# Kernel tuning notes

Measured on AMD Instinct MI355X. Metric: run time of the kernel, lower is better.

## Reference

```python
import jax, jax.numpy as jnp
import numpy as np

B, L, INPUT_DIM = 4, 4096, 32
D_MODEL, N_LAYERS = 256, 2
D_STATE, D_CONV, EXPAND = 16, 4, 2
D_INNER = EXPAND * D_MODEL          # 512
DT_RANK = (D_MODEL + 15) // 16      # 16
OUTPUT_DIM, HORIZON = 32, 4
LN_EPS = 1e-5


def setup_inputs() -> dict:
    key = jax.random.key(0)
    ks = jax.random.split(key, 16)
    s = 0.02
    inp = {
        "x": jax.random.normal(ks[0], (B, L, INPUT_DIM), jnp.float32),
        "enc_w": jax.random.normal(ks[1], (D_MODEL, INPUT_DIM), jnp.float32) * s,
        "enc_b": jnp.zeros((D_MODEL,), jnp.float32),
        "in_proj_w": jax.random.normal(ks[2], (N_LAYERS, 2 * D_INNER, D_MODEL), jnp.float32) * s,
        "conv_w": jax.random.normal(ks[3], (N_LAYERS, D_INNER, D_CONV), jnp.float32) * s,
        "conv_b": jnp.zeros((N_LAYERS, D_INNER), jnp.float32),
        "xproj_w": jax.random.normal(ks[4], (N_LAYERS, DT_RANK + 2 * D_STATE, D_INNER), jnp.float32) * s,
        "dtproj_w": jax.random.normal(ks[5], (N_LAYERS, D_INNER, DT_RANK), jnp.float32) * s,
        "dtproj_b": jax.random.normal(ks[6], (N_LAYERS, D_INNER), jnp.float32) * 0.1,
        "A_log": jnp.log(jnp.tile(jnp.arange(1.0, D_STATE + 1.0, dtype=jnp.float32), (N_LAYERS, D_INNER, 1))),
        "Dp": jnp.ones((N_LAYERS, D_INNER), jnp.float32),
        "out_proj_w": jax.random.normal(ks[7], (N_LAYERS, D_MODEL, D_INNER), jnp.float32) * s,
        "ln_g": jnp.ones((D_MODEL,), jnp.float32),
        "ln_b": jnp.zeros((D_MODEL,), jnp.float32),
        "head_w": jax.random.normal(ks[8], (OUTPUT_DIM * HORIZON, D_MODEL), jnp.float32) * s,
        "head_b": jnp.zeros((OUTPUT_DIM * HORIZON,), jnp.float32),
    }
    return inp


def _mamba_block(x, in_w, cw, cb, xp_w, dt_w, dt_b, A_log, Dp, out_w):
    # x: [B, L, d_model]
    b, l, _ = x.shape
    xz = jnp.einsum("bld,ed->ble", x, in_w)            # [B, L, 2*d_inner]
    xi, res = jnp.split(xz, 2, axis=-1)
    # causal depthwise conv1d (padding=d_conv-1, truncated to L)
    xpad = jnp.pad(xi, ((0, 0), (D_CONV - 1, 0), (0, 0)))
    xi = sum(xpad[:, k:k + l, :] * cw[:, k] for k in range(D_CONV)) + cb
    xi = jax.nn.silu(xi)
    dbl = jnp.einsum("bld,ed->ble", xi, xp_w)           # [B, L, dt_rank+2*d_state]
    dt = dbl[..., :DT_RANK]
    Bm = dbl[..., DT_RANK:DT_RANK + D_STATE]            # [B, L, d_state]
    Cm = dbl[..., DT_RANK + D_STATE:]                   # [B, L, d_state]
    dt = jax.nn.softplus(jnp.einsum("blr,dr->bld", dt, dt_w) + dt_b)  # [B, L, d_inner]
    A = -jnp.exp(A_log)                                 # [d_inner, d_state]

    def step(h, ins):
        dt_t, B_t, C_t, x_t = ins                       # [B,di],[B,ds],[B,ds],[B,di]
        dA = jnp.exp(dt_t[..., None] * A)               # [B, d_inner, d_state]
        h = dA * h + (dt_t * x_t)[..., None] * B_t[:, None, :]
        y = jnp.einsum("bds,bs->bd", h, C_t)
        return h, y

    h0 = jnp.zeros((b, D_INNER, D_STATE), x.dtype)
    xs = (jnp.moveaxis(dt, 1, 0), jnp.moveaxis(Bm, 1, 0),
          jnp.moveaxis(Cm, 1, 0), jnp.moveaxis(xi, 1, 0))
    _, ys = jax.lax.scan(step, h0, xs)                  # ys: [L, B, d_inner]
    y = jnp.moveaxis(ys, 0, 1) + xi * Dp
    y = y * jax.nn.silu(res)
    return jnp.einsum("ble,de->bld", y, out_w)


def reference(x, enc_w, enc_b, in_proj_w, conv_w, conv_b, xproj_w, dtproj_w,
              dtproj_b, A_log, Dp, out_proj_w, ln_g, ln_b, head_w, head_b):
    h = jnp.einsum("bli,di->bld", x, enc_w) + enc_b     # encoder
    for i in range(N_LAYERS):
        h = h + _mamba_block(h, in_proj_w[i], conv_w[i], conv_b[i], xproj_w[i],
                             dtproj_w[i], dtproj_b[i], A_log[i], Dp[i], out_proj_w[i])
    mu = jnp.mean(h, axis=-1, keepdims=True)
    var = jnp.mean((h - mu) ** 2, axis=-1, keepdims=True)
    hn = (h - mu) * jax.lax.rsqrt(var + LN_EPS) * ln_g + ln_b
    state = hn[:, -1, :]                                # last timestep
    return jnp.einsum("bd,od->bo", state, head_w) + head_b
```

## Files before the change

kernel.cpp:

```cpp
#include <hip/hip_runtime.h>
#include <hip/hip_bf16.h>
#include <math.h>

#define BB 4
#define LL 4096
#define DM 256
#define DI 512
#define DS 16
#define NOUTK 128
#define LN_EPS 1e-5f
#define NC 128
#define CLEN (LL/NC)
#define BL (BB*LL)
#define LDB 640

typedef __attribute__((ext_vector_type(8))) short short8;
typedef __attribute__((ext_vector_type(4))) float f32x4;

__device__ __forceinline__ ushort f2bf(float f) {
    union { float f; unsigned u; } v; v.f = f;
    unsigned r = (v.u + 0x7FFF + ((v.u >> 16) & 1)) >> 16;
    return (ushort)r;
}
__device__ __forceinline__ float bf2f(ushort u) {
    union { unsigned u; float f; } v; v.u = ((unsigned)u) << 16;
    return v.f;
}

#define PREP_N1 (2*1024*256)
#define PREP_N2 (2*256*512)
#define PREP_N3 (2*640*512)
#define PREP_BLOCKS ((PREP_N1 + PREP_N2 + PREP_N3) / 256)
#define ENC_BLOCKS (BL / 4)
__global__ __launch_bounds__(256) void prep_enc_kernel(
    const float* __restrict__ inw, const float* __restrict__ opw,
    const float* __restrict__ xpw, const float* __restrict__ dtw,
    ushort* __restrict__ inw_bf, ushort* __restrict__ opw_bf,
    ushort* __restrict__ comb_bf,
    const float* __restrict__ x, const float* __restrict__ encw,
    const float* __restrict__ encb, ushort* __restrict__ hbf)
{
    int tid = threadIdx.x;
    if (blockIdx.x < PREP_BLOCKS) {
        int i = blockIdx.x * 256 + tid;
        if (i < PREP_N1) {
            inw_bf[i] = f2bf(inw[i]);
            return;
        }
        int j = i - PREP_N1;
        if (j < PREP_N2) {
            opw_bf[j] = f2bf(opw[j]);
            return;
        }
        int m = j - PREP_N2;
        if (m >= PREP_N3) return;
        int l = m / (640 * 512);
        int rem = m - l * 640 * 512;
        int row = rem >> 9, k = rem & 511;
        const float* xp = xpw + l * 48 * 512;
        const float* dw = dtw + l * 512 * 16;
        float v;
        if (row < 512) {
            v = 0.f;
            #pragma unroll
            for (int r = 0; r < 16; ++r)
                v = fmaf(dw[row * 16 + r], xp[r * 512 + k], v);
        } else if (row < 544) {
            v = xp[(row - 512 + 16) * 512 + k];
        } else v = 0.f;
        comb_bf[m] = f2bf(v);
        return;
    }
    __shared__ float sw[256 * 33];
    __shared__ float sx[4][32];
    for (int i = tid; i < 256 * 8; i += 256) {
        float4 v = ((const float4*)encw)[i];
        int r = i >> 3, c = (i & 7) * 4;
        sw[r * 33 + c + 0] = v.x; sw[r * 33 + c + 1] = v.y;
        sw[r * 33 + c + 2] = v.z; sw[r * 33 + c + 3] = v.w;
    }
    int row0 = (blockIdx.x - PREP_BLOCKS) * 4;
    if (tid < 32) {
        for (int rr = 0; rr < 4; ++rr)
            sx[rr][tid] = x[(size_t)(row0 + rr) * 32 + tid];
    }
    __syncthreads();
    float bb = encb[tid];
    #pragma unroll
    for (int rr = 0; rr < 4; ++rr) {
        float acc = bb;
        #pragma unroll
        for (int k = 0; k < 32; ++k)
            acc = fmaf(sx[rr][k], sw[tid * 33 + k], acc);
        hbf[(size_t)(row0 + rr) * DM + tid] = f2bf(acc);
    }
}

template<int EPI>
__global__ __launch_bounds__(256, 4) void mfma_gemm(
    const ushort* __restrict__ A, int lda,
    const ushort* __restrict__ W,
    const float* __restrict__ bias,
    float* __restrict__ C, int ldc,
    ushort* Cbf, int ldcbf,
    int K)
{
    __shared__ ushort As[64 * 64];
    __shared__ ushort Ws[128 * 64];
    const int tid = threadIdx.x;

    int nwg = gridDim.x * gridDim.y;
    int wlin = blockIdx.y * gridDim.x + blockIdx.x;
    int gx = blockIdx.x, gy = blockIdx.y;
    if ((nwg & 7) == 0) {
        int q = nwg >> 3;
        int s = (wlin & 7) * q + (wlin >> 3);
        gx = s % gridDim.x;
        gy = s / gridDim.x;
    }
    const int bm = gy * 64;
    const int bn = gx * 128;
    const int wid = tid >> 6, lane = tid & 63;
    const int wrow = (wid >> 1) * 32, wcol = (wid & 1) * 64;
    const int sr = tid >> 3;
    const int sc = tid & 7;

    f32x4 acc[2][4];
    #pragma unroll
    for (int mi = 0; mi < 2; ++mi)
        #pragma unroll
        for (int ni = 0; ni < 4; ++ni)
            acc[mi][ni] = (f32x4){0.f, 0.f, 0.f, 0.f};

    const int nk = K >> 6;
    for (int t = 0; t < nk; ++t) {
        const int k0 = t << 6;
        #pragma unroll
        for (int it = 0; it < 2; ++it) {
            int r = it * 32 + sr;
            int csrc = sc ^ (r & 7);
            __builtin_amdgcn_global_load_lds(
                (const __attribute__((address_space(1))) unsigned int*)
                    (A + (size_t)(bm + r) * lda + k0 + csrc * 8),
                (__attribute__((address_space(3))) unsigned int*)
                    (As + r * 64 + sc * 8), 16, 0, 0);
        }
        #pragma unroll
        for (int it = 0; it < 4; ++it) {
            int r = it * 32 + sr;
            int csrc = sc ^ (r & 7);
            __builtin_amdgcn_global_load_lds(
                (const __attribute__((address_space(1))) unsigned int*)
                    (W + (size_t)(bn + r) * K + k0 + csrc * 8),
                (__attribute__((address_space(3))) unsigned int*)
                    (Ws + r * 64 + sc * 8), 16, 0, 0);
        }
        __syncthreads();
        #pragma unroll
        for (int kk = 0; kk < 2; ++kk) {
            short8 af[2], bfr[4];
            #pragma unroll
            for (int mi = 0; mi < 2; ++mi) {
                int r = wrow + mi * 16 + (lane & 15);
                int c = (lane >> 4) + kk * 4;
                af[mi] = *(const short8*)(As + r * 64 + ((c ^ (r & 7)) << 3));
            }
            #pragma unroll
            for (int ni = 0; ni < 4; ++ni) {
                int r = wcol + ni * 16 + (lane & 15);
                int c = (lane >> 4) + kk * 4;
                bfr[ni] = *(const short8*)(Ws + r * 64 + ((c ^ (r & 7)) << 3));
            }
            #pragma unroll
            for (int mi = 0; mi < 2; ++mi)
                #pragma unroll
                for (int ni = 0; ni < 4; ++ni)
                    acc[mi][ni] = __builtin_amdgcn_mfma_f32_16x16x32_bf16(
                        af[mi], bfr[ni], acc[mi][ni], 0, 0, 0);
        }
        __syncthreads();
    }

    #pragma unroll
    for (int mi = 0; mi < 2; ++mi)
        #pragma unroll
        for (int ni = 0; ni < 4; ++ni) {
            int col = bn + wcol + ni * 16 + (lane & 15);
            #pragma unroll
            for (int r = 0; r < 4; ++r) {
                int row = bm + wrow + mi * 16 + (lane >> 4) * 4 + r;
                float v = acc[mi][ni][r];
                if (EPI == 1) {
                    if (col < 512) {
                        float u = v + bias[col];
                        float sp = fmaxf(u, 0.f) + __logf(1.f + __expf(-fabsf(u)));
                        Cbf[(size_t)row * ldcbf + col] = f2bf(sp);
                    } else if (col < 544) {
                        C[(size_t)row * ldc + (col - 512)] = v;
                    }
                } else if (EPI == 2) {
                    size_t o = (size_t)row * ldcbf + col;
                    float vv = v + bf2f(Cbf[o]);
                    Cbf[o] = f2bf(vv);
                } else {
                    Cbf[(size_t)row * ldcbf + col] = f2bf(v);
                }
            }
        }
}

__global__ __launch_bounds__(256) void conv_silu_kernel(
    const ushort* __restrict__ xz, const float* __restrict__ cw,
    const float* __restrict__ cb, ushort* __restrict__ xi)
{
    int idx = blockIdx.x * 256 + threadIdx.x;
    int d4 = (idx & 127) * 4;
    int grp = idx >> 7;
    int b = grp >> 9;
    int t0 = (grp & 511) * 8;
    const ushort* base = xz + ((size_t)(b * LL + t0) * 1024) + d4;
    ushort* obase = xi + ((size_t)(b * LL + t0) * 512) + d4;

    float4 w0 = *(const float4*)(cw + (d4 + 0) * 4);
    float4 w1 = *(const float4*)(cw + (d4 + 1) * 4);
    float4 w2 = *(const float4*)(cw + (d4 + 2) * 4);
    float4 w3 = *(const float4*)(cw + (d4 + 3) * 4);
    float b0 = cb[d4 + 0], b1 = cb[d4 + 1], b2 = cb[d4 + 2], b3 = cb[d4 + 3];

    ushort4 z4 = {0, 0, 0, 0};
    ushort4 win0 = (t0 >= 3) ? *(const ushort4*)(base - 3 * 1024) : z4;
    ushort4 win1 = (t0 >= 2) ? *(const ushort4*)(base - 2 * 1024) : z4;
    ushort4 win2 = (t0 >= 1) ? *(const ushort4*)(base - 1 * 1024) : z4;

    #pragma unroll
    for (int k = 0; k < 8; ++k) {
        ushort4 cur = *(const ushort4*)(base + k * 1024);
        float a0 = b0, a1 = b1, a2 = b2, a3 = b3;
        a0 = fmaf(bf2f(win0.x), w0.x, a0); a1 = fmaf(bf2f(win0.y), w1.x, a1);
        a2 = fmaf(bf2f(win0.z), w2.x, a2); a3 = fmaf(bf2f(win0.w), w3.x, a3);
        a0 = fmaf(bf2f(win1.x), w0.y, a0); a1 = fmaf(bf2f(win1.y), w1.y, a1);
        a2 = fmaf(bf2f(win1.z), w2.y, a2); a3 = fmaf(bf2f(win1.w), w3.y, a3);
        a0 = fmaf(bf2f(win2.x), w0.z, a0); a1 = fmaf(bf2f(win2.y), w1.z, a1);
        a2 = fmaf(bf2f(win2.z), w2.z, a2); a3 = fmaf(bf2f(win2.w), w3.z, a3);
        a0 = fmaf(bf2f(cur.x),  w0.w, a0); a1 = fmaf(bf2f(cur.y),  w1.w, a1);
        a2 = fmaf(bf2f(cur.z),  w2.w, a2); a3 = fmaf(bf2f(cur.w),  w3.w, a3);
        ushort4 o;
        o.x = f2bf(a0 / (1.f + __expf(-a0)));
        o.y = f2bf(a1 / (1.f + __expf(-a1)));
        o.z = f2bf(a2 / (1.f + __expf(-a2)));
        o.w = f2bf(a3 / (1.f + __expf(-a3)));
        *(ushort4*)(obase + k * 512) = o;
        win0 = win1; win1 = win2; win2 = cur;
    }
}

__global__ __launch_bounds__(256) void scan_phase1(
    const ushort* __restrict__ xi, const ushort* __restrict__ dtb,
    const float* __restrict__ bc,
    const float* __restrict__ alog,
    float* __restrict__ cS, float* __restrict__ cH)
{
    int d = blockIdx.z * 256 + threadIdx.x;
    int b = blockIdx.y, c = blockIdx.x;
    float Av[16];
    bool fast = true;
    #pragma unroll
    for (int s = 0; s < 16; ++s) {
        Av[s] = -__expf(alog[d * 16 + s]);
        fast = fast && (fabsf(Av[s] + (float)(s + 1)) < 1e-3f * (s + 1));
    }
    float h[16];
    #pragma unroll
    for (int s = 0; s < 16; ++s) h[s] = 0.f;
    float S = 0.f;
    int t0 = c * CLEN;
    if (fast) {
        for (int t = t0; t < t0 + CLEN; ++t) {
            size_t row = (size_t)b * LL + t;
            float dt = bf2f(dtb[row * 512 + d]);
            float x = bf2f(xi[row * 512 + d]);
            float dtx = dt * x;
            S += dt;
            const float* bp = bc + row * 32;
            float e1 = __expf(-dt);
            float e2=e1*e1, e3=e2*e1, e4=e2*e2, e5=e3*e2, e6=e3*e3, e7=e4*e3, e8=e4*e4;
            float e9=e5*e4, e10=e5*e5, e11=e6*e5, e12=e6*e6, e13=e7*e6, e14=e7*e7, e15=e8*e7, e16=e8*e8;
            float pw[16] = {e1,e2,e3,e4,e5,e6,e7,e8,e9,e10,e11,e12,e13,e14,e15,e16};
            #pragma unroll
            for (int s = 0; s < 16; ++s)
                h[s] = fmaf(pw[s], h[s], dtx * bp[s]);
        }
    } else {
        for (int t = t0; t < t0 + CLEN; ++t) {
            size_t row = (size_t)b * LL + t;
            float dt = bf2f(dtb[row * 512 + d]);
            float x = bf2f(xi[row * 512 + d]);
            float dtx = dt * x;
            S += dt;
            const float* bp = bc + row * 32;
            #pragma unroll
            for (int s = 0; s < 16; ++s) {
                float dA = __expf(dt * Av[s]);
                h[s] = fmaf(dA, h[s], dtx * bp[s]);
            }
        }
    }
    cS[((size_t)b * DI + d) * NC + c] = S;
    size_t base = (((size_t)b * DI + d) * NC + c) * 16;
    #pragma unroll
    for (int q = 0; q < 4; ++q)
        *(float4*)(cH + base + q*4) = *(float4*)&h[q*4];
}

__global__ __launch_bounds__(256) void scan_phase2(
    const float* __restrict__ cS, float* __restrict__ cH,
    const float* __restrict__ alog)
{
    int bd = blockIdx.x;
    int d = bd & (DI - 1);
    int tid = threadIdx.x;
    int s = tid >> 4;
    int g = tid & 15;
    float Avs = -__expf(alog[d * 16 + s]);
    size_t sbase = (size_t)bd * NC;
    size_t base = (size_t)bd * NC * 16 + s;
    float a8[8], h8[8];
    #pragma unroll
    for (int j = 0; j < 8; ++j) {
        float Sj = cS[sbase + g * 8 + j];
        a8[j] = __expf(Avs * Sj);
        h8[j] = cH[base + (size_t)(g * 8 + j) * 16];
    }
    float A = 1.f, H = 0.f;
    #pragma unroll
    for (int j = 0; j < 8; ++j) {
        H = fmaf(a8[j], H, h8[j]);
        A *= a8[j];
    }
    #pragma unroll
    for (int off = 1; off < 16; off <<= 1) {
        float Ap = __shfl_up(A, off, 16);
        float Hp = __shfl_up(H, off, 16);
        if (g >= off) { H = fmaf(A, Hp, H); A *= Ap; }
    }
    float init = __shfl_up(H, 1, 16);
    if (g == 0) init = 0.f;
    #pragma unroll
    for (int j = 0; j < 8; ++j) {
        size_t o = base + (size_t)(g * 8 + j) * 16;
        cH[o] = init;
        init = fmaf(a8[j], init, h8[j]);
    }
}

__global__ __launch_bounds__(256) void scan_phase3(
    const ushort* __restrict__ xz,
    ushort* __restrict__ xi,
    const ushort* __restrict__ dtb,
    const float* __restrict__ bc,
    const float* __restrict__ alog,
    const float* __restrict__ Dp,
    const float* __restrict__ cH,
    int c0)
{
    int d = blockIdx.z * 256 + threadIdx.x;
    int b = blockIdx.y;
    int c = blockIdx.x + c0;
    float Av[16];
    bool fast = true;
    #pragma unroll
    for (int s = 0; s < 16; ++s) {
        Av[s] = -__expf(alog[d * 16 + s]);
        fast = fast && (fabsf(Av[s] + (float)(s + 1)) < 1e-3f * (s + 1));
    }
    float h[16];
    size_t cbase = (((size_t)b * DI + d) * NC + c) * 16;
    #pragma unroll
    for (int q = 0; q < 4; ++q)
        *(float4*)&h[q*4] = *(const float4*)(cH + cbase + q*4);
    float Dd = Dp[d];
    int t0 = c * CLEN;
    if (fast) {
        for (int t = t0; t < t0 + CLEN; ++t) {
            size_t row = (size_t)b * LL + t;
            float dt = bf2f(dtb[row * 512 + d]);
            float x = bf2f(xi[row * 512 + d]);
            float dtx = dt * x;
            const float* bp = bc + row * 32;
            const float* cp = bc + row * 32 + 16;
            float e1 = __expf(-dt);
            float e2=e1*e1, e3=e2*e1, e4=e2*e2, e5=e3*e2, e6=e3*e3, e7=e4*e3, e8=e4*e4;
            float e9=e5*e4, e10=e5*e5, e11=e6*e5, e12=e6*e6, e13=e7*e6, e14=e7*e7, e15=e8*e7, e16=e8*e8;
            float pw[16] = {e1,e2,e3,e4,e5,e6,e7,e8,e9,e10,e11,e12,e13,e14,e15,e16};
            float y = 0.f;
            #pragma unroll
            for (int s = 0; s < 16; ++s) {
                h[s] = fmaf(pw[s], h[s], dtx * bp[s]);
                y = fmaf(h[s], cp[s], y);
            }
            float res = bf2f(xz[row * 1024 + 512 + d]);
            float g = (y + x * Dd) * (res / (1.f + __expf(-res)));
            xi[row * 512 + d] = f2bf(g);
        }
    } else {
        for (int t = t0; t < t0 + CLEN; ++t) {
            size_t row = (size_t)b * LL + t;
            float dt = bf2f(dtb[row * 512 + d]);
            float x = bf2f(xi[row * 512 + d]);
            float dtx = dt * x;
            const float* bp = bc + row * 32;
            const float* cp = bc + row * 32 + 16;
            float y = 0.f;
            #pragma unroll
            for (int s = 0; s < 16; ++s) {
                float dA = __expf(dt * Av[s]);
                h[s] = fmaf(dA, h[s], dtx * bp[s]);
                y = fmaf(h[s], cp[s], y);
            }
            float res = bf2f(xz[row * 1024 + 512 + d]);
            float g = (y + x * Dd) * (res / (1.f + __expf(-res)));
            xi[row * 512 + d] = f2bf(g);
        }
    }
}

__global__ __launch_bounds__(256) void out_proj_last_kernel(
    const ushort* __restrict__ xi, const float* __restrict__ W,
    const ushort* __restrict__ hbf, float* __restrict__ hlast)
{
    int b = blockIdx.x, n = threadIdx.x;
    __shared__ float sy[DI];
    const ushort* yrow = xi + ((size_t)b * LL + (LL - 1)) * DI;
    for (int k = threadIdx.x; k < DI; k += 256) sy[k] = bf2f(yrow[k]);
    __syncthreads();
    const float* wr = W + (size_t)n * DI;
    float acc = 0.f;
    for (int k = 0; k < DI; k += 4) {
        float4 wv = *(const float4*)(wr + k);
        acc = fmaf(sy[k+0], wv.x, acc);
        acc = fmaf(sy[k+1], wv.y, acc);
        acc = fmaf(sy[k+2], wv.z, acc);
        acc = fmaf(sy[k+3], wv.w, acc);
    }
    hlast[b * DM + n] = acc + bf2f(hbf[((size_t)b * LL + (LL - 1)) * DM + n]);
}

__global__ __launch_bounds__(256) void ln_head_kernel(
    const float* __restrict__ hlast, const float* __restrict__ lng,
    const float* __restrict__ lnb, const float* __restrict__ hw,
    const float* __restrict__ hb, float* __restrict__ out)
{
    int b = blockIdx.x, tid = threadIdx.x;
    __shared__ float sh[DM];
    __shared__ float r1[4], r2[4];
    float v = hlast[b * DM + tid];
    float s = v;
    #pragma unroll
    for (int o = 32; o >= 1; o >>= 1) s += __shfl_down(s, o);
    if ((tid & 63) == 0) r1[tid >> 6] = s;
    __syncthreads();
    float mu = (r1[0] + r1[1] + r1[2] + r1[3]) * (1.f / 256.f);
    float dv = v - mu;
    float q = dv * dv;
    #pragma unroll
    for (int o = 32; o >= 1; o >>= 1) q += __shfl_down(q, o);
    if ((tid & 63) == 0) r2[tid >> 6] = q;
    __syncthreads();
    float var = (r2[0] + r2[1] + r2[2] + r2[3]) * (1.f / 256.f);
    sh[tid] = dv * rsqrtf(var + LN_EPS) * lng[tid] + lnb[tid];
    __syncthreads();
    if (tid < NOUTK) {
        const float* wr = hw + (size_t)tid * DM;
        float acc = hb[tid];
        for (int d2 = 0; d2 < DM; d2 += 4) {
            float4 wv = *(const float4*)(wr + d2);
            acc = fmaf(sh[d2+0], wv.x, acc);
            acc = fmaf(sh[d2+1], wv.y, acc);
            acc = fmaf(sh[d2+2], wv.z, acc);
            acc = fmaf(sh[d2+3], wv.w, acc);
        }
        out[b * NOUTK + tid] = acc;
    }
}

extern "C" void kernel_launch(void* const* d_in, const int* in_sizes, int n_in,
                              void* d_out, int out_size, void* d_ws, size_t ws_size,
                              hipStream_t stream)
{
    const float* x    = (const float*)d_in[0];
    const float* encw = (const float*)d_in[1];
    const float* encb = (const float*)d_in[2];
    const float* inw  = (const float*)d_in[3];
    const float* cw   = (const float*)d_in[4];
    const float* cb   = (const float*)d_in[5];
    const float* xpw  = (const float*)d_in[6];
    const float* dtw  = (const float*)d_in[7];
    const float* dtb  = (const float*)d_in[8];
    const float* alog = (const float*)d_in[9];
    const float* Dp   = (const float*)d_in[10];
    const float* opw  = (const float*)d_in[11];
    const float* lng  = (const float*)d_in[12];
    const float* lnb  = (const float*)d_in[13];
    const float* hw   = (const float*)d_in[14];
    const float* hb   = (const float*)d_in[15];
    float* out = (float*)d_out;

    float* ws   = (float*)d_ws;
    float* bc   = ws;
    float* cS   = bc  + (size_t)BL * 32;
    float* cH   = cS  + (size_t)BB * DI * NC;
    float* hlast = cH + (size_t)BB * DI * NC * DS;
    ushort* h_bf    = (ushort*)(hlast + BB * DM);
    ushort* xz_bf   = h_bf  + (size_t)BL * DM;
    ushort* xi_bf   = xz_bf + (size_t)BL * 1024;
    ushort* dt_bf   = xi_bf + (size_t)BL * DI;
    ushort* inw_bf  = dt_bf + (size_t)BL * DI;
    ushort* opw_bf  = inw_bf + 2 * 1024 * DM;
    ushort* comb_bf = opw_bf + 2 * DM * DI;

    dim3 blk(256, 1, 1);

    prep_enc_kernel<<<dim3(PREP_BLOCKS + ENC_BLOCKS), blk, 0, stream>>>(
        inw, opw, xpw, dtw, inw_bf, opw_bf, comb_bf,
        x, encw, encb, h_bf);

    for (int l = 0; l < 2; ++l) {
        mfma_gemm<0><<<dim3(1024/128, BL/64), blk, 0, stream>>>(
            h_bf, DM, inw_bf + (size_t)l * 1024 * DM, nullptr,
            nullptr, 0, xz_bf, 1024, DM);
        conv_silu_kernel<<<dim3(BL * 128 / 8 / 256), blk, 0, stream>>>(
            xz_bf, cw + l * DI * 4, cb + l * DI, xi_bf);
        mfma_gemm<1><<<dim3(LDB/128, BL/64), blk, 0, stream>>>(
            xi_bf, DI, comb_bf + (size_t)l * LDB * DI, dtb + l * DI,
            bc, 32, dt_bf, 512, DI);
        scan_phase1<<<dim3(NC, BB, 2), blk, 0, stream>>>(
            xi_bf, dt_bf, bc, alog + (size_t)l * DI * 16, cS, cH);
        scan_phase2<<<dim3(BB * DI), blk, 0, stream>>>(
            cS, cH, alog + (size_t)l * DI * 16);
        if (l == 0) {
            scan_phase3<<<dim3(NC, BB, 2), blk, 0, stream>>>(
                xz_bf, xi_bf, dt_bf, bc, alog + (size_t)l * DI * 16,
                Dp + l * DI, cH, 0);
            mfma_gemm<2><<<dim3(DM/128, BL/64), blk, 0, stream>>>(
                xi_bf, DI, opw_bf + (size_t)l * DM * DI, nullptr,
                nullptr, 0, h_bf, DM, DI);
        } else {
            scan_phase3<<<dim3(1, BB, 2), blk, 0, stream>>>(
                xz_bf, xi_bf, dt_bf, bc, alog + (size_t)l * DI * 16,
                Dp + l * DI, cH, NC - 1);
            out_proj_last_kernel<<<dim3(BB), blk, 0, stream>>>(
                xi_bf, opw + (size_t)l * DM * DI, h_bf, hlast);
        }
    }

    ln_head_kernel<<<dim3(BB), blk, 0, stream>>>(hlast, lng, lnb, hw, hb, out);
}
```

Baseline: 307.1 us.

## Unfuse dt low-rank projection: small x_proj GEMM plus separate dt combine

```diff
diff --git a/kernel.cpp b/kernel.cpp
--- a/kernel.cpp
+++ b/kernel.cpp
@@ -12,7 +12,6 @@
 #define NC 128
 #define CLEN (LL/NC)
 #define BL (BB*LL)
-#define LDB 640
 
 typedef __attribute__((ext_vector_type(8))) short short8;
 typedef __attribute__((ext_vector_type(4))) float f32x4;
@@ -29,14 +28,14 @@
 
 #define PREP_N1 (2*1024*256)
 #define PREP_N2 (2*256*512)
-#define PREP_N3 (2*640*512)
+#define PREP_N3 (2*64*512)
 #define PREP_BLOCKS ((PREP_N1 + PREP_N2 + PREP_N3) / 256)
 #define ENC_BLOCKS (BL / 4)
 __global__ __launch_bounds__(256) void prep_enc_kernel(
     const float* __restrict__ inw, const float* __restrict__ opw,
-    const float* __restrict__ xpw, const float* __restrict__ dtw,
+    const float* __restrict__ xpw,
     ushort* __restrict__ inw_bf, ushort* __restrict__ opw_bf,
-    ushort* __restrict__ comb_bf,
+    ushort* __restrict__ xpw48_bf,
     const float* __restrict__ x, const float* __restrict__ encw,
     const float* __restrict__ encb, ushort* __restrict__ hbf)
 {
@@ -54,21 +53,11 @@
         }
         int m = j - PREP_N2;
         if (m >= PREP_N3) return;
-        int l = m / (640 * 512);
-        int rem = m - l * 640 * 512;
+        int l = m / (64 * 512);
+        int rem = m - l * 64 * 512;
         int row = rem >> 9, k = rem & 511;
-        const float* xp = xpw + l * 48 * 512;
-        const float* dw = dtw + l * 512 * 16;
-        float v;
-        if (row < 512) {
-            v = 0.f;
-            #pragma unroll
-            for (int r = 0; r < 16; ++r)
-                v = fmaf(dw[row * 16 + r], xp[r * 512 + k], v);
-        } else if (row < 544) {
-            v = xp[(row - 512 + 16) * 512 + k];
-        } else v = 0.f;
-        comb_bf[m] = f2bf(v);
+        float v = (row < 48) ? xpw[(size_t)l * 48 * 512 + row * 512 + k] : 0.f;
+        xpw48_bf[m] = f2bf(v);
         return;
     }
     __shared__ float sw[256 * 33];
@@ -100,8 +89,6 @@
 __global__ __launch_bounds__(256, 4) void mfma_gemm(
     const ushort* __restrict__ A, int lda,
     const ushort* __restrict__ W,
-    const float* __restrict__ bias,
-    float* __restrict__ C, int ldc,
     ushort* Cbf, int ldcbf,
     int K)
 {
@@ -190,15 +177,7 @@
             for (int r = 0; r < 4; ++r) {
                 int row = bm + wrow + mi * 16 + (lane >> 4) * 4 + r;
                 float v = acc[mi][ni][r];
-                if (EPI == 1) {
-                    if (col < 512) {
-                        float u = v + bias[col];
-                        float sp = fmaxf(u, 0.f) + __logf(1.f + __expf(-fabsf(u)));
-                        Cbf[(size_t)row * ldcbf + col] = f2bf(sp);
-                    } else if (col < 544) {
-                        C[(size_t)row * ldc + (col - 512)] = v;
-                    }
-                } else if (EPI == 2) {
+                if (EPI == 2) {
                     size_t o = (size_t)row * ldcbf + col;
                     float vv = v + bf2f(Cbf[o]);
                     Cbf[o] = f2bf(vv);
@@ -207,6 +186,123 @@
                 }
             }
         }
+}
+
+__global__ __launch_bounds__(256, 4) void mfma_gemm48(
+    const ushort* __restrict__ A,
+    const ushort* __restrict__ W,
+    float* __restrict__ r16,
+    float* __restrict__ bc)
+{
+    __shared__ ushort As[64 * 64];
+    __shared__ ushort Ws[64 * 64];
+    const int tid = threadIdx.x;
+
+    int nwg = gridDim.y;
+    int wlin = blockIdx.y;
+    int gy = wlin;
+    if ((nwg & 7) == 0) {
+        int q = nwg >> 3;
+        gy = (wlin & 7) * q + (wlin >> 3);
+    }
+    const int bm = gy * 64;
+    const int wid = tid >> 6, lane = tid & 63;
+    const int wrow = wid * 16;
+    const int sr = tid >> 3;
+    const int sc = tid & 7;
+
+    f32x4 acc[4];
+    #pragma unroll
+    for (int ni = 0; ni < 4; ++ni)
+        acc[ni] = (f32x4){0.f, 0.f, 0.f, 0.f};
+
+    for (int t = 0; t < 8; ++t) {
+        const int k0 = t << 6;
+        #pragma unroll
+        for (int it = 0; it < 2; ++it) {
+            int r = it * 32 + sr;
+            int csrc = sc ^ (r & 7);
+            __builtin_amdgcn_global_load_lds(
+                (const __attribute__((address_space(1))) unsigned int*)
+                    (A + (size_t)(bm + r) * DI + k0 + csrc * 8),
+                (__attribute__((address_space(3))) unsigned int*)
+                    (As + r * 64 + sc * 8), 16, 0, 0);
+        }
+        #pragma unroll
+        for (int it = 0; it < 2; ++it) {
+            int r = it * 32 + sr;
+            int csrc = sc ^ (r & 7);
+            __builtin_amdgcn_global_load_lds(
+                (const __attribute__((address_space(1))) unsigned int*)
+                    (W + (size_t)r * DI + k0 + csrc * 8),
+                (__attribute__((address_space(3))) unsigned int*)
+                    (Ws + r * 64 + sc * 8), 16, 0, 0);
+        }
+        __syncthreads();
+        #pragma unroll
+        for (int kk = 0; kk < 2; ++kk) {
+            int c = (lane >> 4) + kk * 4;
+            int ra = wrow + (lane & 15);
+            short8 af = *(const short8*)(As + ra * 64 + ((c ^ (ra & 7)) << 3));
+            #pragma unroll
+            for (int ni = 0; ni < 4; ++ni) {
+                int rb = ni * 16 + (lane & 15);
+                short8 bfr = *(const short8*)(Ws + rb * 64 + ((c ^ (rb & 7)) << 3));
+                acc[ni] = __builtin_amdgcn_mfma_f32_16x16x32_bf16(
+                    af, bfr, acc[ni], 0, 0, 0);
+            }
+        }
+        __syncthreads();
+    }
+
+    #pragma unroll
+    for (int ni = 0; ni < 3; ++ni) {
+        int col = ni * 16 + (lane & 15);
+        #pragma unroll
+        for (int r = 0; r < 4; ++r) {
+            int row = bm + wrow + (lane >> 4) * 4 + r;
+            float v = acc[ni][r];
+            if (col < 16) r16[(size_t)row * 16 + col] = v;
+            else          bc[(size_t)row * 32 + (col - 16)] = v;
+        }
+    }
+}
+
+__global__ __launch_bounds__(256) void dt_combine_kernel(
+    const float* __restrict__ r16, const float* __restrict__ dtw,
+    const float* __restrict__ dtb, ushort* __restrict__ dt_bf)
+{
+    int idx = blockIdx.x * 256 + threadIdx.x;
+    int n0 = (idx & 127) * 4;
+    int row = idx >> 7;
+    const float* rp = r16 + (size_t)row * 16;
+    float4 ra = *(const float4*)(rp + 0);
+    float4 rb = *(const float4*)(rp + 4);
+    float4 rc = *(const float4*)(rp + 8);
+    float4 rd = *(const float4*)(rp + 12);
+    ushort4 o;
+    #pragma unroll
+    for (int j = 0; j < 4; ++j) {
+        const float* w = dtw + (size_t)(n0 + j) * 16;
+        float4 wa = *(const float4*)(w + 0);
+        float4 wb = *(const float4*)(w + 4);
+        float4 wc = *(const float4*)(w + 8);
+        float4 wd = *(const float4*)(w + 12);
+        float acc = dtb[n0 + j];
+        acc = fmaf(ra.x, wa.x, acc); acc = fmaf(ra.y, wa.y, acc);
+        acc = fmaf(ra.z, wa.z, acc); acc = fmaf(ra.w, wa.w, acc);
+        acc = fmaf(rb.x, wb.x, acc); acc = fmaf(rb.y, wb.y, acc);
+        acc = fmaf(rb.z, wb.z, acc); acc = fmaf(rb.w, wb.w, acc);
+        acc = fmaf(rc.x, wc.x, acc); acc = fmaf(rc.y, wc.y, acc);
+        acc = fmaf(rc.z, wc.z, acc); acc = fmaf(rc.w, wc.w, acc);
+        acc = fmaf(rd.x, wd.x, acc); acc = fmaf(rd.y, wd.y, acc);
+        acc = fmaf(rd.z, wd.z, acc); acc = fmaf(rd.w, wd.w, acc);
+        float sp = fmaxf(acc, 0.f) + __logf(1.f + __expf(-fabsf(acc)));
+        ushort u = f2bf(sp);
+        if (j == 0) o.x = u; else if (j == 1) o.y = u;
+        else if (j == 2) o.z = u; else o.w = u;
+    }
+    *(ushort4*)(dt_bf + (size_t)row * 512 + n0) = o;
 }
 
 __global__ __launch_bounds__(256) void conv_silu_kernel(
@@ -509,30 +605,32 @@
     float* bc   = ws;
     float* cS   = bc  + (size_t)BL * 32;
     float* cH   = cS  + (size_t)BB * DI * NC;
-    float* hlast = cH + (size_t)BB * DI * NC * DS;
+    float* r16  = cH  + (size_t)BB * DI * NC * DS;
+    float* hlast = r16 + (size_t)BL * 16;
     ushort* h_bf    = (ushort*)(hlast + BB * DM);
     ushort* xz_bf   = h_bf  + (size_t)BL * DM;
     ushort* xi_bf   = xz_bf + (size_t)BL * 1024;
     ushort* dt_bf   = xi_bf + (size_t)BL * DI;
     ushort* inw_bf  = dt_bf + (size_t)BL * DI;
     ushort* opw_bf  = inw_bf + 2 * 1024 * DM;
-    ushort* comb_bf = opw_bf + 2 * DM * DI;
+    ushort* xpw48_bf = opw_bf + 2 * DM * DI;
 
     dim3 blk(256, 1, 1);
 
     prep_enc_kernel<<<dim3(PREP_BLOCKS + ENC_BLOCKS), blk, 0, stream>>>(
-        inw, opw, xpw, dtw, inw_bf, opw_bf, comb_bf,
+        inw, opw, xpw, inw_bf, opw_bf, xpw48_bf,
         x, encw, encb, h_bf);
 
     for (int l = 0; l < 2; ++l) {
         mfma_gemm<0><<<dim3(1024/128, BL/64), blk, 0, stream>>>(
-            h_bf, DM, inw_bf + (size_t)l * 1024 * DM, nullptr,
-            nullptr, 0, xz_bf, 1024, DM);
+            h_bf, DM, inw_bf + (size_t)l * 1024 * DM,
+            xz_bf, 1024, DM);
         conv_silu_kernel<<<dim3(BL * 128 / 8 / 256), blk, 0, stream>>>(
             xz_bf, cw + l * DI * 4, cb + l * DI, xi_bf);
-        mfma_gemm<1><<<dim3(LDB/128, BL/64), blk, 0, stream>>>(
-            xi_bf, DI, comb_bf + (size_t)l * LDB * DI, dtb + l * DI,
-            bc, 32, dt_bf, 512, DI);
+        mfma_gemm48<<<dim3(1, BL/64), blk, 0, stream>>>(
+            xi_bf, xpw48_bf + (size_t)l * 64 * DI, r16, bc);
+        dt_combine_kernel<<<dim3(BL * 128 / 256), blk, 0, stream>>>(
+            r16, dtw + (size_t)l * DI * 16, dtb + (size_t)l * DI, dt_bf);
         scan_phase1<<<dim3(NC, BB, 2), blk, 0, stream>>>(
             xi_bf, dt_bf, bc, alog + (size_t)l * DI * 16, cS, cH);
         scan_phase2<<<dim3(BB * DI), blk, 0, stream>>>(
@@ -542,8 +640,8 @@
                 xz_bf, xi_bf, dt_bf, bc, alog + (size_t)l * DI * 16,
                 Dp + l * DI, cH, 0);
             mfma_gemm<2><<<dim3(DM/128, BL/64), blk, 0, stream>>>(
-                xi_bf, DI, opw_bf + (size_t)l * DM * DI, nullptr,
-                nullptr, 0, h_bf, DM, DI);
+                xi_bf, DI, opw_bf + (size_t)l * DM * DI,
+                h_bf, DM, DI);
         } else {
             scan_phase3<<<dim3(1, BB, 2), blk, 0, stream>>>(
                 xz_bf, xi_bf, dt_bf, bc, alog + (size_t)l * DI * 16,
```

After: 400.3 us. 1.3x slower.
